# Performance work log

Hardware: AMD Instinct MI355X
Metric: run time of the kernel (lower is better)

The kernel has to match this reference:

```python
import jax, jax.numpy as jnp
import numpy as np
import math

B, T, D = 2, 2048, 2048
H, HKV, HD = 16, 4, 128
THETA = 10000.0


def _rope_tables(seq_len, head_dim, theta):
    inv_freq = 1.0 / theta ** (jnp.arange(0, head_dim, 2, dtype=jnp.float32) / head_dim)
    t = jnp.arange(seq_len, dtype=jnp.float32)
    freqs = jnp.outer(t, inv_freq)  # (T, HD/2)
    return jnp.cos(freqs), jnp.sin(freqs)


def _apply_rope(x, cos, sin):
    # x: (B, h, T, HD); cos/sin: (T, HD/2)
    hd = x.shape[-1]
    x1, x2 = x[..., : hd // 2], x[..., hd // 2 :]
    rotated = jnp.concatenate([-x2, x1], axis=-1)
    c = jnp.concatenate([cos, cos], axis=-1)[None, None]  # (1,1,T,HD)
    s = jnp.concatenate([sin, sin], axis=-1)[None, None]
    return x * c + rotated * s


def setup_inputs() -> dict:
    key = jax.random.key(0)
    ks = jax.random.split(key, 5)
    sc = 0.02
    return {
        "x": jax.random.normal(ks[0], (B, T, D), dtype=jnp.float32),
        "attention_mask": jnp.ones((B, T), dtype=jnp.int32),
        "causal": 1,
        "wq": jax.random.normal(ks[1], (D, H * HD), dtype=jnp.float32) * sc,
        "wk": jax.random.normal(ks[2], (D, HKV * HD), dtype=jnp.float32) * sc,
        "wv": jax.random.normal(ks[3], (D, HKV * HD), dtype=jnp.float32) * sc,
        "wo": jax.random.normal(ks[4], (D, D), dtype=jnp.float32) * sc,
    }


def reference(x, attention_mask, causal, wq, wk, wv, wo):
    b, t, d = x.shape
    G = H // HKV  # query heads per kv head

    q = (x @ wq).reshape(b, t, H, HD).transpose(0, 2, 1, 3)      # (B,H,T,HD)
    k = (x @ wk).reshape(b, t, HKV, HD).transpose(0, 2, 1, 3)    # (B,HKV,T,HD)
    v = (x @ wv).reshape(b, t, HKV, HD).transpose(0, 2, 1, 3)

    cos, sin = _rope_tables(t, HD, THETA)
    q = _apply_rope(q, cos, sin)
    k = _apply_rope(k, cos, sin)

    # group queries so repeat_interleave of k/v is implicit
    qg = q.reshape(b, HKV, G, t, HD)
    scores = jnp.einsum("bkgtd,bksd->bkgts", qg, k) / math.sqrt(HD)

    key_pad = (attention_mask == 0)[:, None, None, None, :]  # (B,1,1,1,T)
    scores = jnp.where(key_pad, -jnp.inf, scores)
    if causal:
        cm = jnp.triu(jnp.ones((t, t), dtype=bool), k=1)
        scores = jnp.where(cm[None, None, None], -jnp.inf, scores)

    attn = jax.nn.softmax(scores, axis=-1)  # dropout p=0.0 -> identity in eval
    out = jnp.einsum("bkgts,bksd->bkgtd", attn, v)            # (B,HKV,G,T,HD)
    out = out.reshape(b, H, t, HD).transpose(0, 2, 1, 3).reshape(b, t, H * HD)
    return out @ wo
```

## Files before the change

### kernel.cpp

```cpp
#include <hip/hip_runtime.h>
#include <hip/hip_bf16.h>
#include <stdint.h>

#define B_    2
#define T_    2048
#define D_    2048
#define H_    16
#define HKV_  4
#define HD_   128
#define BT_   (B_ * T_)
#define QD_   2048
#define KVD_  512

typedef float  f32x4 __attribute__((ext_vector_type(4)));
typedef short  s16x8 __attribute__((ext_vector_type(8)));
typedef unsigned short us;

__device__ __forceinline__ us f2bf(float f) {
    unsigned int u = __builtin_bit_cast(unsigned int, f);
    u += 0x7FFFu + ((u >> 16) & 1u);
    return (us)(u >> 16);
}
__device__ __forceinline__ float bf2f(us s) {
    unsigned int u = ((unsigned int)s) << 16;
    return __builtin_bit_cast(float, u);
}
__device__ __forceinline__ unsigned pack2(float a, float b) {
    return (unsigned)f2bf(a) | ((unsigned)f2bf(b) << 16);
}

#define GLOBAL_AS __attribute__((address_space(1)))
#define LDS_AS    __attribute__((address_space(3)))

__device__ __forceinline__ void gload16(const void* g, void* l) {
    __builtin_amdgcn_global_load_lds((const GLOBAL_AS uint32_t*)g,
                                     (LDS_AS uint32_t*)l, 16, 0, 0);
}

__global__ __launch_bounds__(256)
void wtrans(const float* __restrict__ w, us* __restrict__ wt, int K, int N) {
    __shared__ float t[32][33];
    const int k0 = blockIdx.x * 32, n0 = blockIdx.y * 32;
    const int tid = threadIdx.x;
    const int r = tid >> 3, c4 = (tid & 7) << 2;
    const float4 v = *(const float4*)&w[(size_t)(k0 + r) * N + n0 + c4];
    t[r][c4 + 0] = v.x; t[r][c4 + 1] = v.y; t[r][c4 + 2] = v.z; t[r][c4 + 3] = v.w;
    __syncthreads();
    ushort4 o;
    o.x = f2bf(t[c4 + 0][r]); o.y = f2bf(t[c4 + 1][r]);
    o.z = f2bf(t[c4 + 2][r]); o.w = f2bf(t[c4 + 3][r]);
    *(ushort4*)&wt[(size_t)(n0 + r) * K + k0 + c4] = o;
}

__global__ __launch_bounds__(256)
void cvt_bf16(const float* __restrict__ x, us* __restrict__ xb, int n8) {
    const int i = blockIdx.x * 256 + threadIdx.x;
    if (i >= n8) return;
    const float4 a = ((const float4*)x)[i * 2];
    const float4 b = ((const float4*)x)[i * 2 + 1];
    s16x8 o;
    o[0] = (short)f2bf(a.x); o[1] = (short)f2bf(a.y);
    o[2] = (short)f2bf(a.z); o[3] = (short)f2bf(a.w);
    o[4] = (short)f2bf(b.x); o[5] = (short)f2bf(b.y);
    o[6] = (short)f2bf(b.z); o[7] = (short)f2bf(b.w);
    *(s16x8*)&xb[(size_t)i * 8] = o;
}

__global__ __launch_bounds__(256)
void build_tabs(float* __restrict__ tab, float* __restrict__ bias,
                const int* __restrict__ amask) {
    const int i = blockIdx.x * 256 + threadIdx.x;
    if (i < T_ * 64) {
        const int t = i >> 6, f = i & 63;
        const float inv = __expf((float)f * (-0.14391156642478335f));
        float s, c;
        sincosf((float)t * inv, &s, &c);
        tab[t * 128 + f] = c;
        tab[t * 128 + 64 + f] = s;
    }
    if (i < B_ * T_) bias[i] = amask[i] ? 0.f : -__builtin_inff();
}

template <int NH>
__global__ __launch_bounds__(256)
void rope_apply(us* __restrict__ x, const float* __restrict__ tab, int total4) {
    const int idx = blockIdx.x * 256 + threadIdx.x;
    if (idx >= total4) return;
    const int i0  = (idx & 15) << 2;
    const int rest = idx >> 4;
    const int h   = rest % NH;
    const int row = rest / NH;
    const int t   = row & (T_ - 1);
    const f32x4 c = *(const f32x4*)&tab[t * 128 + i0];
    const f32x4 s = *(const f32x4*)&tab[t * 128 + 64 + i0];
    const size_t base = (size_t)row * (NH * 128) + h * 128 + i0;
    ushort4 lo = *(ushort4*)&x[base];
    ushort4 hi = *(ushort4*)&x[base + 64];
    float x1[4] = {bf2f(lo.x), bf2f(lo.y), bf2f(lo.z), bf2f(lo.w)};
    float x2[4] = {bf2f(hi.x), bf2f(hi.y), bf2f(hi.z), bf2f(hi.w)};
    ushort4 olo, ohi;
    olo.x = f2bf(x1[0]*c[0] - x2[0]*s[0]); ohi.x = f2bf(x2[0]*c[0] + x1[0]*s[0]);
    olo.y = f2bf(x1[1]*c[1] - x2[1]*s[1]); ohi.y = f2bf(x2[1]*c[1] + x1[1]*s[1]);
    olo.z = f2bf(x1[2]*c[2] - x2[2]*s[2]); ohi.z = f2bf(x2[2]*c[2] + x1[2]*s[2]);
    olo.w = f2bf(x1[3]*c[3] - x2[3]*s[3]); ohi.w = f2bf(x2[3]*c[3] + x1[3]*s[3]);
    *(ushort4*)&x[base]      = olo;
    *(ushort4*)&x[base + 64] = ohi;
}

template <bool AF32, int OUTMODE>
__global__ __launch_bounds__(256)
void gemm_bf16(const void* __restrict__ Ap, const us* __restrict__ Bt,
               void* __restrict__ Cp, int M, int N, int K) {
    __shared__ us As[128 * 32];
    __shared__ us Bs[128 * 32];

    const int tid  = threadIdx.x;
    const int lane = tid & 63;
    const int w    = tid >> 6;
    const int lrow = lane & 15;
    const int lhi  = lane >> 4;
    const int wm   = w >> 1;
    const int wn   = w & 1;
    const int mbase = blockIdx.y * 128;
    const int nbase = blockIdx.x * 128;

    f32x4 acc[4][4] = {};

    for (int k0 = 0; k0 < K; k0 += 32) {
        __syncthreads();
        if constexpr (AF32) {
            const float* A = (const float*)Ap;
#pragma unroll
            for (int i = 0; i < 2; ++i) {
                const int c   = tid * 2 + i;
                const int row = c >> 2, cc = c & 3;
                const float* src = A + (size_t)(mbase + row) * K + k0 + ((cc ^ (row & 3)) << 3);
                const float4 v0 = *(const float4*)src;
                const float4 v1 = *(const float4*)(src + 4);
                s16x8 o;
                o[0] = (short)f2bf(v0.x); o[1] = (short)f2bf(v0.y);
                o[2] = (short)f2bf(v0.z); o[3] = (short)f2bf(v0.w);
                o[4] = (short)f2bf(v1.x); o[5] = (short)f2bf(v1.y);
                o[6] = (short)f2bf(v1.z); o[7] = (short)f2bf(v1.w);
                *(s16x8*)&As[c * 8] = o;
            }
        } else {
            const us* A = (const us*)Ap;
#pragma unroll
            for (int i = 0; i < 2; ++i) {
                const int cb = i * 256 + w * 64;
                const int c  = cb + lane;
                const int row = c >> 2, cc = c & 3;
                gload16(A + (size_t)(mbase + row) * K + k0 + ((cc ^ (row & 3)) << 3),
                        &As[cb * 8]);
            }
        }
#pragma unroll
        for (int i = 0; i < 2; ++i) {
            const int cb = i * 256 + w * 64;
            const int c  = cb + lane;
            const int row = c >> 2, cc = c & 3;
            gload16(Bt + (size_t)(nbase + row) * K + k0 + ((cc ^ (row & 3)) << 3),
                    &Bs[cb * 8]);
        }
        __syncthreads();

        s16x8 af[4], bfv[4];
#pragma unroll
        for (int mi = 0; mi < 4; ++mi) {
            const int r = wm * 64 + mi * 16 + lrow;
            af[mi] = *(const s16x8*)&As[r * 32 + ((lhi ^ (r & 3)) << 3)];
        }
#pragma unroll
        for (int ni = 0; ni < 4; ++ni) {
            const int r = wn * 64 + ni * 16 + lrow;
            bfv[ni] = *(const s16x8*)&Bs[r * 32 + ((lhi ^ (r & 3)) << 3)];
        }
#pragma unroll
        for (int mi = 0; mi < 4; ++mi)
#pragma unroll
            for (int ni = 0; ni < 4; ++ni)
                acc[mi][ni] = __builtin_amdgcn_mfma_f32_16x16x32_bf16(
                    af[mi], bfv[ni], acc[mi][ni], 0, 0, 0);
    }

#pragma unroll
    for (int mi = 0; mi < 4; ++mi) {
#pragma unroll
        for (int ni = 0; ni < 4; ++ni) {
#pragma unroll
            for (int r = 0; r < 4; ++r) {
                const int gm = mbase + wm * 64 + mi * 16 + lhi * 4 + r;
                const int gn = nbase + wn * 64 + ni * 16 + lrow;
                const float v = acc[mi][ni][r];
                if constexpr (OUTMODE == 0) {
                    ((us*)Cp)[(size_t)gm * N + gn] = f2bf(v);
                } else if constexpr (OUTMODE == 1) {
                    ((float*)Cp)[(size_t)gm * N + gn] = v;
                } else {
                    const int b = gm >> 11, t = gm & (T_ - 1);
                    if (gn < KVD_) {
                        ((us*)Cp)[(size_t)gm * KVD_ + gn] = f2bf(v);
                    } else {
                        const int nv = gn - KVD_;
                        us* vt = (us*)Cp + (size_t)BT_ * KVD_;
                        vt[((size_t)(b * HKV_ + (nv >> 7)) * 128 + (nv & 127)) * T_ + t] = f2bf(v);
                    }
                }
            }
        }
    }
}

__global__ __launch_bounds__(256)
void attn_mfma2(const us* __restrict__ qg, const us* __restrict__ kg,
                const us* __restrict__ vtg, const float* __restrict__ bias,
                const int* __restrict__ causal_p, us* __restrict__ outg) {
    __shared__ us lds[32768];

    const int q0 = blockIdx.x * 64;
    const int h  = blockIdx.y;
    const int b  = blockIdx.z;
    const int kvh = h >> 2;
    const int causal = *causal_p;
    const int tid  = threadIdx.x;
    const int lane = tid & 63;
    const int w    = tid >> 6;
    const int lrow = lane & 15, lhi = lane >> 4;

    auto stageKV = [&](int buf, int s0) {
        us* Kd = lds + buf * 8192;
        us* Vd = lds + 16384 + buf * 8192;
#pragma unroll
        for (int i = 0; i < 4; ++i) {
            const int cb = i * 256 + w * 64;
            const int c  = cb + lane;
            const int row = c >> 4, cc = c & 15;
            gload16(kg + (size_t)(b * T_ + s0 + row) * KVD_ + kvh * HD_ + ((cc ^ (row & 7)) << 3),
                    Kd + cb * 8);
        }
#pragma unroll
        for (int i = 0; i < 4; ++i) {
            const int cb = i * 256 + w * 64;
            const int c  = cb + lane;
            const int row = c >> 3, cc = c & 7;
            gload16(vtg + (size_t)((b * HKV_ + kvh) * 128 + row) * T_ + s0 + ((cc ^ (row & 7)) << 3),
                    Vd + cb * 8);
        }
    };

#pragma unroll
    for (int i = 0; i < 4; ++i) {
        const int cb = i * 256 + w * 64;
        const int c  = cb + lane;
        const int row = c >> 4, cc = c & 15;
        gload16(qg + (size_t)(b * T_ + q0 + row) * QD_ + h * HD_ + ((cc ^ (row & 7)) << 3),
                lds + 8192 + cb * 8);
    }
    __syncthreads();

    s16x8 qf[4];
    {
        const us* Qsp = lds + 8192;
        const int qr = w * 16 + lrow;
#pragma unroll
        for (int kc = 0; kc < 4; ++kc)
            qf[kc] = *(const s16x8*)&Qsp[qr * 128 + (((kc * 4 + lhi) ^ (qr & 7)) << 3)];
    }
    stageKV(0, 0);
    __syncthreads();

    f32x4 o[8] = {};
    float m_run = -__builtin_inff();
    float l_run = 0.f;
    const int qp = q0 + w * 16 + lrow;
    const int smax = causal ? (q0 + 64) : T_;
    const int ntiles = smax >> 6;
    const float rscale = 0.08838834764831845f;
    int cur = 0;

    for (int it = 0; it < ntiles; ++it) {
        const int s0 = it << 6;
        if (it + 1 < ntiles) stageKV(cur ^ 1, s0 + 64);

        const us* Kcur = lds + cur * 8192;
        const us* Vcur = lds + 16384 + cur * 8192;

        f32x4 sf[4];
#pragma unroll
        for (int j = 0; j < 4; ++j) {
            f32x4 s = {0.f, 0.f, 0.f, 0.f};
            const int kr = j * 16 + lrow;
#pragma unroll
            for (int kc = 0; kc < 4; ++kc) {
                const s16x8 kf = *(const s16x8*)&Kcur[kr * 128 + (((kc * 4 + lhi) ^ (kr & 7)) << 3)];
                s = __builtin_amdgcn_mfma_f32_16x16x32_bf16(kf, qf[kc], s, 0, 0, 0);
            }
            sf[j] = s;
        }

        const float* brow = bias + b * T_ + s0;
        f32x4 bv[4];
#pragma unroll
        for (int j = 0; j < 4; ++j)
            bv[j] = *(const f32x4*)&brow[j * 16 + lhi * 4];
        const bool needc = causal && (s0 + 63 > q0 + w * 16);
        float x[4][4];
#pragma unroll
        for (int j = 0; j < 4; ++j)
#pragma unroll
            for (int r = 0; r < 4; ++r) {
                float xv = sf[j][r] * rscale + bv[j][r];
                if (needc && (s0 + j * 16 + lhi * 4 + r > qp)) xv = -__builtin_inff();
                x[j][r] = xv;
            }

        float tmax = x[0][0];
#pragma unroll
        for (int j = 0; j < 4; ++j)
#pragma unroll
            for (int r = 0; r < 4; ++r) tmax = fmaxf(tmax, x[j][r]);
        tmax = fmaxf(tmax, __shfl_xor(tmax, 16));
        tmax = fmaxf(tmax, __shfl_xor(tmax, 32));
        const float mn = fmaxf(m_run, tmax);
        float corr, ls = 0.f, ps[4][4];
        if (mn == -__builtin_inff()) {
            corr = 1.f;
#pragma unroll
            for (int j = 0; j < 4; ++j)
#pragma unroll
                for (int r = 0; r < 4; ++r) ps[j][r] = 0.f;
        } else {
            corr = __expf(m_run - mn);
#pragma unroll
            for (int j = 0; j < 4; ++j)
#pragma unroll
                for (int r = 0; r < 4; ++r) { ps[j][r] = __expf(x[j][r] - mn); ls += ps[j][r]; }
        }
        ls += __shfl_xor(ls, 16);
        ls += __shfl_xor(ls, 32);
        l_run = l_run * corr + ls;
        m_run = mn;

        const unsigned w00 = pack2(ps[0][0], ps[0][1]), w01 = pack2(ps[0][2], ps[0][3]);
        const unsigned w10 = pack2(ps[1][0], ps[1][1]), w11 = pack2(ps[1][2], ps[1][3]);
        const unsigned w20 = pack2(ps[2][0], ps[2][1]), w21 = pack2(ps[2][2], ps[2][3]);
        const unsigned w30 = pack2(ps[3][0], ps[3][1]), w31 = pack2(ps[3][2], ps[3][3]);
        int a0w[4], a1w[4];
#pragma unroll
        for (int m = 0; m < 4; ++m) {
            const int src = lrow + ((lhi & 1) << 5) + ((m & 2) << 3);
            const unsigned c0 = (m & 1) ? w01 : w00;
            const unsigned c1 = (m & 1) ? w11 : w10;
            const int t0 = __shfl((int)c0, src);
            const int t1 = __shfl((int)c1, src);
            a0w[m] = (lhi & 2) ? t1 : t0;
            const unsigned c2 = (m & 1) ? w21 : w20;
            const unsigned c3 = (m & 1) ? w31 : w30;
            const int t2 = __shfl((int)c2, src);
            const int t3 = __shfl((int)c3, src);
            a1w[m] = (lhi & 2) ? t3 : t2;
        }
        const s16x8 a0 = __builtin_bit_cast(s16x8, make_int4(a0w[0], a0w[1], a0w[2], a0w[3]));
        const s16x8 a1 = __builtin_bit_cast(s16x8, make_int4(a1w[0], a1w[1], a1w[2], a1w[3]));

        float co[4];
#pragma unroll
        for (int r = 0; r < 4; ++r) co[r] = __shfl(corr, lhi * 4 + r);
#pragma unroll
        for (int dc = 0; dc < 8; ++dc) {
            o[dc][0] *= co[0]; o[dc][1] *= co[1];
            o[dc][2] *= co[2]; o[dc][3] *= co[3];
        }
#pragma unroll
        for (int dc = 0; dc < 8; ++dc) {
            const int vr = dc * 16 + lrow;
            const s16x8 vb0 = *(const s16x8*)&Vcur[vr * 64 + ((lhi ^ (vr & 7)) << 3)];
            o[dc] = __builtin_amdgcn_mfma_f32_16x16x32_bf16(a0, vb0, o[dc], 0, 0, 0);
            const s16x8 vb1 = *(const s16x8*)&Vcur[vr * 64 + (((4 + lhi) ^ (vr & 7)) << 3)];
            o[dc] = __builtin_amdgcn_mfma_f32_16x16x32_bf16(a1, vb1, o[dc], 0, 0, 0);
        }
        __syncthreads();
        cur ^= 1;
    }

    float lq[4];
#pragma unroll
    for (int r = 0; r < 4; ++r) lq[r] = __shfl(l_run, lhi * 4 + r);
#pragma unroll
    for (int r = 0; r < 4; ++r) {
        const float invl = lq[r] > 0.f ? 1.0f / lq[r] : 0.f;
        const size_t base = (size_t)(b * T_ + q0 + w * 16 + lhi * 4 + r) * QD_ + h * HD_ + lrow;
#pragma unroll
        for (int dc = 0; dc < 8; ++dc)
            outg[base + dc * 16] = f2bf(o[dc][r] * invl);
    }
}

extern "C" void kernel_launch(void* const* d_in, const int* in_sizes, int n_in,
                              void* d_out, int out_size, void* d_ws, size_t ws_size,
                              hipStream_t stream) {
    const float* x      = (const float*)d_in[0];
    const int*   amask  = (const int*)d_in[1];
    const int*   causal = (const int*)d_in[2];
    const float* wq     = (const float*)d_in[3];
    const float* wk     = (const float*)d_in[4];
    const float* wv     = (const float*)d_in[5];
    const float* wo     = (const float*)d_in[6];
    float* out = (float*)d_out;

    us* p    = (us*)d_ws;
    us* wqt  = p;  p += (size_t)QD_ * D_;
    us* wkvt = p;  p += (size_t)1024 * D_;
    us* qb   = p;  p += (size_t)BT_ * QD_;
    us* kb   = p;  p += (size_t)BT_ * KVD_;
    us* vt   = p;  p += (size_t)BT_ * KVD_;
    float* tab  = (float*)p;  p += (size_t)T_ * 128 * 2;
    float* bias = (float*)p;  p += (size_t)B_ * T_ * 2;
    us* xw   = p;

    const size_t need_xb = ((size_t)(p - (us*)d_ws) + (size_t)BT_ * D_) * sizeof(us);
    const bool useXB = ws_size >= need_xb;

    build_tabs<<<512, 256, 0, stream>>>(tab, bias, amask);
    wtrans<<<dim3(64, 64), 256, 0, stream>>>(wq, wqt, D_, QD_);
    wtrans<<<dim3(64, 16), 256, 0, stream>>>(wk, wkvt, D_, KVD_);
    wtrans<<<dim3(64, 16), 256, 0, stream>>>(wv, wkvt + (size_t)KVD_ * D_, D_, KVD_);

    if (useXB) {
        cvt_bf16<<<4096, 256, 0, stream>>>(x, xw, BT_ * D_ / 8);
        gemm_bf16<false, 0><<<dim3(16, 32), 256, 0, stream>>>(xw, wqt, qb, BT_, QD_, D_);
        gemm_bf16<false, 2><<<dim3(8, 32), 256, 0, stream>>>(xw, wkvt, kb, BT_, 1024, D_);
    } else {
        gemm_bf16<true, 0><<<dim3(16, 32), 256, 0, stream>>>(x, wqt, qb, BT_, QD_, D_);
        gemm_bf16<true, 2><<<dim3(8, 32), 256, 0, stream>>>(x, wkvt, kb, BT_, 1024, D_);
    }

    rope_apply<H_><<<4096, 256, 0, stream>>>(qb, tab, BT_ * H_ * 16);
    rope_apply<HKV_><<<1024, 256, 0, stream>>>(kb, tab, BT_ * HKV_ * 16);

    attn_mfma2<<<dim3(32, 16, 2), 256, 0, stream>>>(qb, kb, vt, bias, causal, qb);

    wtrans<<<dim3(64, 64), 256, 0, stream>>>(wo, xw, D_, D_);
    gemm_bf16<false, 1><<<dim3(16, 32), 256, 0, stream>>>(qb, xw, out, BT_, D_, D_);
}
```

Before: 458.2 us.

## Double attention query tile to 128 rows with deferred rescale and LDS P transpose

```diff
diff --git a/kernel.cpp b/kernel.cpp
--- a/kernel.cpp
+++ b/kernel.cpp
@@ -188,24 +188,29 @@
     for (int mi = 0; mi < 4; ++mi) {
 #pragma unroll
         for (int ni = 0; ni < 4; ++ni) {
-#pragma unroll
-            for (int r = 0; r < 4; ++r) {
-                const int gm = mbase + wm * 64 + mi * 16 + lhi * 4 + r;
-                const int gn = nbase + wn * 64 + ni * 16 + lrow;
-                const float v = acc[mi][ni][r];
-                if constexpr (OUTMODE == 0) {
-                    ((us*)Cp)[(size_t)gm * N + gn] = f2bf(v);
-                } else if constexpr (OUTMODE == 1) {
-                    ((float*)Cp)[(size_t)gm * N + gn] = v;
+            const int gm0 = mbase + wm * 64 + mi * 16 + lhi * 4;
+            const int gn  = nbase + wn * 64 + ni * 16 + lrow;
+            if constexpr (OUTMODE == 0) {
+#pragma unroll
+                for (int r = 0; r < 4; ++r)
+                    ((us*)Cp)[(size_t)(gm0 + r) * N + gn] = f2bf(acc[mi][ni][r]);
+            } else if constexpr (OUTMODE == 1) {
+#pragma unroll
+                for (int r = 0; r < 4; ++r)
+                    ((float*)Cp)[(size_t)(gm0 + r) * N + gn] = acc[mi][ni][r];
+            } else {
+                if (gn < KVD_) {
+#pragma unroll
+                    for (int r = 0; r < 4; ++r)
+                        ((us*)Cp)[(size_t)(gm0 + r) * KVD_ + gn] = f2bf(acc[mi][ni][r]);
                 } else {
-                    const int b = gm >> 11, t = gm & (T_ - 1);
-                    if (gn < KVD_) {
-                        ((us*)Cp)[(size_t)gm * KVD_ + gn] = f2bf(v);
-                    } else {
-                        const int nv = gn - KVD_;
-                        us* vt = (us*)Cp + (size_t)BT_ * KVD_;
-                        vt[((size_t)(b * HKV_ + (nv >> 7)) * 128 + (nv & 127)) * T_ + t] = f2bf(v);
-                    }
+                    const int nv = gn - KVD_;
+                    const int bb = gm0 >> 11, t = gm0 & (T_ - 1);
+                    us* vt = (us*)Cp + (size_t)BT_ * KVD_;
+                    ushort4 o4;
+                    o4.x = f2bf(acc[mi][ni][0]); o4.y = f2bf(acc[mi][ni][1]);
+                    o4.z = f2bf(acc[mi][ni][2]); o4.w = f2bf(acc[mi][ni][3]);
+                    *(ushort4*)&vt[((size_t)(bb * HKV_ + (nv >> 7)) * 128 + (nv & 127)) * T_ + t] = o4;
                 }
             }
         }
@@ -213,12 +218,13 @@
 }
 
 __global__ __launch_bounds__(256)
-void attn_mfma2(const us* __restrict__ qg, const us* __restrict__ kg,
+void attn_mfma3(const us* __restrict__ qg, const us* __restrict__ kg,
                 const us* __restrict__ vtg, const float* __restrict__ bias,
                 const int* __restrict__ causal_p, us* __restrict__ outg) {
-    __shared__ us lds[32768];
-
-    const int q0 = blockIdx.x * 64;
+    __shared__ us lds[40960];
+
+    const int qt = 15 - blockIdx.x;
+    const int q0 = qt * 128;
     const int h  = blockIdx.y;
     const int b  = blockIdx.z;
     const int kvh = h >> 2;
@@ -250,32 +256,34 @@
     };
 
 #pragma unroll
-    for (int i = 0; i < 4; ++i) {
+    for (int i = 0; i < 8; ++i) {
         const int cb = i * 256 + w * 64;
         const int c  = cb + lane;
         const int row = c >> 4, cc = c & 15;
+        us* dst = (cb < 1024) ? (lds + 8192 + cb * 8) : (lds + 24576 + (cb - 1024) * 8);
         gload16(qg + (size_t)(b * T_ + q0 + row) * QD_ + h * HD_ + ((cc ^ (row & 7)) << 3),
-                lds + 8192 + cb * 8);
+                dst);
     }
     __syncthreads();
 
-    s16x8 qf[4];
-    {
-        const us* Qsp = lds + 8192;
-        const int qr = w * 16 + lrow;
+    s16x8 qf[2][4];
+#pragma unroll
+    for (int s = 0; s < 2; ++s) {
+        const int qr = w * 32 + s * 16 + lrow;
+        const us* Qsp = (w * 32 + s * 16 < 64) ? (lds + 8192 + qr * 128)
+                                               : (lds + 24576 + (qr - 64) * 128);
 #pragma unroll
         for (int kc = 0; kc < 4; ++kc)
-            qf[kc] = *(const s16x8*)&Qsp[qr * 128 + (((kc * 4 + lhi) ^ (qr & 7)) << 3)];
+            qf[s][kc] = *(const s16x8*)&Qsp[((kc * 4 + lhi) ^ (qr & 7)) << 3];
     }
     stageKV(0, 0);
     __syncthreads();
 
-    f32x4 o[8] = {};
-    float m_run = -__builtin_inff();
-    float l_run = 0.f;
-    const int qp = q0 + w * 16 + lrow;
-    const int smax = causal ? (q0 + 64) : T_;
-    const int ntiles = smax >> 6;
+    f32x4 o[2][8] = {};
+    float m_run[2] = {-__builtin_inff(), -__builtin_inff()};
+    float l_run[2] = {0.f, 0.f};
+    us* Pw = lds + 32768 + w * 2048;
+    const int ntiles = (causal ? (q0 + 128) : T_) >> 6;
     const float rscale = 0.08838834764831845f;
     int cur = 0;
 
@@ -286,17 +294,18 @@
         const us* Kcur = lds + cur * 8192;
         const us* Vcur = lds + 16384 + cur * 8192;
 
-        f32x4 sf[4];
+        f32x4 sf[2][4];
 #pragma unroll
         for (int j = 0; j < 4; ++j) {
-            f32x4 s = {0.f, 0.f, 0.f, 0.f};
+            f32x4 a0 = {0.f, 0.f, 0.f, 0.f}, a1 = {0.f, 0.f, 0.f, 0.f};
             const int kr = j * 16 + lrow;
 #pragma unroll
             for (int kc = 0; kc < 4; ++kc) {
                 const s16x8 kf = *(const s16x8*)&Kcur[kr * 128 + (((kc * 4 + lhi) ^ (kr & 7)) << 3)];
-                s = __builtin_amdgcn_mfma_f32_16x16x32_bf16(kf, qf[kc], s, 0, 0, 0);
-            }
-            sf[j] = s;
+                a0 = __builtin_amdgcn_mfma_f32_16x16x32_bf16(kf, qf[0][kc], a0, 0, 0, 0);
+                a1 = __builtin_amdgcn_mfma_f32_16x16x32_bf16(kf, qf[1][kc], a1, 0, 0, 0);
+            }
+            sf[0][j] = a0; sf[1][j] = a1;
         }
 
         const float* brow = bias + b * T_ + s0;
@@ -304,96 +313,108 @@
 #pragma unroll
         for (int j = 0; j < 4; ++j)
             bv[j] = *(const f32x4*)&brow[j * 16 + lhi * 4];
-        const bool needc = causal && (s0 + 63 > q0 + w * 16);
-        float x[4][4];
-#pragma unroll
-        for (int j = 0; j < 4; ++j)
-#pragma unroll
-            for (int r = 0; r < 4; ++r) {
-                float xv = sf[j][r] * rscale + bv[j][r];
-                if (needc && (s0 + j * 16 + lhi * 4 + r > qp)) xv = -__builtin_inff();
-                x[j][r] = xv;
-            }
-
-        float tmax = x[0][0];
-#pragma unroll
-        for (int j = 0; j < 4; ++j)
-#pragma unroll
-            for (int r = 0; r < 4; ++r) tmax = fmaxf(tmax, x[j][r]);
-        tmax = fmaxf(tmax, __shfl_xor(tmax, 16));
-        tmax = fmaxf(tmax, __shfl_xor(tmax, 32));
-        const float mn = fmaxf(m_run, tmax);
-        float corr, ls = 0.f, ps[4][4];
-        if (mn == -__builtin_inff()) {
-            corr = 1.f;
+
+        s16x8 pa[2][2];
+#pragma unroll
+        for (int s = 0; s < 2; ++s) {
+            const int qp = q0 + w * 32 + s * 16 + lrow;
+            const bool needc = causal && (s0 + 63 > q0 + w * 32 + s * 16);
+            float x[4][4];
 #pragma unroll
             for (int j = 0; j < 4; ++j)
 #pragma unroll
-                for (int r = 0; r < 4; ++r) ps[j][r] = 0.f;
-        } else {
-            corr = __expf(m_run - mn);
+                for (int r = 0; r < 4; ++r) {
+                    float xv = sf[s][j][r] * rscale + bv[j][r];
+                    if (needc && (s0 + j * 16 + lhi * 4 + r > qp)) xv = -__builtin_inff();
+                    x[j][r] = xv;
+                }
+
+            float tmax = x[0][0];
 #pragma unroll
             for (int j = 0; j < 4; ++j)
 #pragma unroll
-                for (int r = 0; r < 4; ++r) { ps[j][r] = __expf(x[j][r] - mn); ls += ps[j][r]; }
-        }
-        ls += __shfl_xor(ls, 16);
-        ls += __shfl_xor(ls, 32);
-        l_run = l_run * corr + ls;
-        m_run = mn;
-
-        const unsigned w00 = pack2(ps[0][0], ps[0][1]), w01 = pack2(ps[0][2], ps[0][3]);
-        const unsigned w10 = pack2(ps[1][0], ps[1][1]), w11 = pack2(ps[1][2], ps[1][3]);
-        const unsigned w20 = pack2(ps[2][0], ps[2][1]), w21 = pack2(ps[2][2], ps[2][3]);
-        const unsigned w30 = pack2(ps[3][0], ps[3][1]), w31 = pack2(ps[3][2], ps[3][3]);
-        int a0w[4], a1w[4];
-#pragma unroll
-        for (int m = 0; m < 4; ++m) {
-            const int src = lrow + ((lhi & 1) << 5) + ((m & 2) << 3);
-            const unsigned c0 = (m & 1) ? w01 : w00;
-            const unsigned c1 = (m & 1) ? w11 : w10;
-            const int t0 = __shfl((int)c0, src);
-            const int t1 = __shfl((int)c1, src);
-            a0w[m] = (lhi & 2) ? t1 : t0;
-            const unsigned c2 = (m & 1) ? w21 : w20;
-            const unsigned c3 = (m & 1) ? w31 : w30;
-            const int t2 = __shfl((int)c2, src);
-            const int t3 = __shfl((int)c3, src);
-            a1w[m] = (lhi & 2) ? t3 : t2;
-        }
-        const s16x8 a0 = __builtin_bit_cast(s16x8, make_int4(a0w[0], a0w[1], a0w[2], a0w[3]));
-        const s16x8 a1 = __builtin_bit_cast(s16x8, make_int4(a1w[0], a1w[1], a1w[2], a1w[3]));
-
-        float co[4];
-#pragma unroll
-        for (int r = 0; r < 4; ++r) co[r] = __shfl(corr, lhi * 4 + r);
-#pragma unroll
-        for (int dc = 0; dc < 8; ++dc) {
-            o[dc][0] *= co[0]; o[dc][1] *= co[1];
-            o[dc][2] *= co[2]; o[dc][3] *= co[3];
-        }
+                for (int r = 0; r < 4; ++r) tmax = fmaxf(tmax, x[j][r]);
+            tmax = fmaxf(tmax, __shfl_xor(tmax, 16));
+            tmax = fmaxf(tmax, __shfl_xor(tmax, 32));
+
+            const bool defer = (m_run[s] != -__builtin_inff()) &&
+                               __all(tmax <= m_run[s] + 8.f);
+            float corr = 1.f, ls = 0.f;
+            float ps[4][4];
+            if (defer) {
+                const float mo = m_run[s];
+#pragma unroll
+                for (int j = 0; j < 4; ++j)
+#pragma unroll
+                    for (int r = 0; r < 4; ++r) { ps[j][r] = __expf(x[j][r] - mo); ls += ps[j][r]; }
+            } else {
+                const float mn = fmaxf(m_run[s], tmax);
+                if (mn == -__builtin_inff()) {
+#pragma unroll
+                    for (int j = 0; j < 4; ++j)
+#pragma unroll
+                        for (int r = 0; r < 4; ++r) ps[j][r] = 0.f;
+                } else {
+                    corr = __expf(m_run[s] - mn);
+#pragma unroll
+                    for (int j = 0; j < 4; ++j)
+#pragma unroll
+                        for (int r = 0; r < 4; ++r) { ps[j][r] = __expf(x[j][r] - mn); ls += ps[j][r]; }
+                }
+                float co[4];
+#pragma unroll
+                for (int r = 0; r < 4; ++r) co[r] = __shfl(corr, lhi * 4 + r);
+#pragma unroll
+                for (int dc = 0; dc < 8; ++dc) {
+                    o[s][dc][0] *= co[0]; o[s][dc][1] *= co[1];
+                    o[s][dc][2] *= co[2]; o[s][dc][3] *= co[3];
+                }
+                m_run[s] = mn;
+            }
+            ls += __shfl_xor(ls, 16);
+            ls += __shfl_xor(ls, 32);
+            l_run[s] = l_run[s] * corr + ls;
+
+            us* Ps = Pw + s * 1024;
+#pragma unroll
+            for (int j = 0; j < 4; ++j) {
+                uint2 wv;
+                wv.x = pack2(ps[j][0], ps[j][1]);
+                wv.y = pack2(ps[j][2], ps[j][3]);
+                *(uint2*)&Ps[lrow * 64 + ((16 * j + 4 * lhi) ^ ((lrow & 7) << 3))] = wv;
+            }
+            pa[s][0] = *(const s16x8*)&Ps[lrow * 64 + ((8 * lhi) ^ ((lrow & 7) << 3))];
+            pa[s][1] = *(const s16x8*)&Ps[lrow * 64 + ((32 + 8 * lhi) ^ ((lrow & 7) << 3))];
+        }
+
 #pragma unroll
         for (int dc = 0; dc < 8; ++dc) {
             const int vr = dc * 16 + lrow;
             const s16x8 vb0 = *(const s16x8*)&Vcur[vr * 64 + ((lhi ^ (vr & 7)) << 3)];
-            o[dc] = __builtin_amdgcn_mfma_f32_16x16x32_bf16(a0, vb0, o[dc], 0, 0, 0);
             const s16x8 vb1 = *(const s16x8*)&Vcur[vr * 64 + (((4 + lhi) ^ (vr & 7)) << 3)];
-            o[dc] = __builtin_amdgcn_mfma_f32_16x16x32_bf16(a1, vb1, o[dc], 0, 0, 0);
+            o[0][dc] = __builtin_amdgcn_mfma_f32_16x16x32_bf16(pa[0][0], vb0, o[0][dc], 0, 0, 0);
+            o[0][dc] = __builtin_amdgcn_mfma_f32_16x16x32_bf16(pa[0][1], vb1, o[0][dc], 0, 0, 0);
+            o[1][dc] = __builtin_amdgcn_mfma_f32_16x16x32_bf16(pa[1][0], vb0, o[1][dc], 0, 0, 0);
+            o[1][dc] = __builtin_amdgcn_mfma_f32_16x16x32_bf16(pa[1][1], vb1, o[1][dc], 0, 0, 0);
         }
         __syncthreads();
         cur ^= 1;
     }
 
-    float lq[4];
-#pragma unroll
-    for (int r = 0; r < 4; ++r) lq[r] = __shfl(l_run, lhi * 4 + r);
-#pragma unroll
-    for (int r = 0; r < 4; ++r) {
-        const float invl = lq[r] > 0.f ? 1.0f / lq[r] : 0.f;
-        const size_t base = (size_t)(b * T_ + q0 + w * 16 + lhi * 4 + r) * QD_ + h * HD_ + lrow;
-#pragma unroll
-        for (int dc = 0; dc < 8; ++dc)
-            outg[base + dc * 16] = f2bf(o[dc][r] * invl);
+#pragma unroll
+    for (int s = 0; s < 2; ++s) {
+        float lq[4];
+#pragma unroll
+        for (int r = 0; r < 4; ++r) lq[r] = __shfl(l_run[s], lhi * 4 + r);
+#pragma unroll
+        for (int r = 0; r < 4; ++r) {
+            const float invl = lq[r] > 0.f ? 1.0f / lq[r] : 0.f;
+            const size_t base =
+                (size_t)(b * T_ + q0 + w * 32 + s * 16 + lhi * 4 + r) * QD_ + h * HD_ + lrow;
+#pragma unroll
+            for (int dc = 0; dc < 8; ++dc)
+                outg[base + dc * 16] = f2bf(o[s][dc][r] * invl);
+        }
     }
 }
 
@@ -439,7 +460,7 @@
     rope_apply<H_><<<4096, 256, 0, stream>>>(qb, tab, BT_ * H_ * 16);
     rope_apply<HKV_><<<1024, 256, 0, stream>>>(kb, tab, BT_ * HKV_ * 16);
 
-    attn_mfma2<<<dim3(32, 16, 2), 256, 0, stream>>>(qb, kb, vt, bias, causal, qb);
+    attn_mfma3<<<dim3(16, 16, 2), 256, 0, stream>>>(qb, kb, vt, bias, causal, qb);
 
     wtrans<<<dim3(64, 64), 256, 0, stream>>>(wo, xw, D_, D_);
     gemm_bf16<false, 1><<<dim3(16, 32), 256, 0, stream>>>(qb, xw, out, BT_, D_, D_);
```

Measured after the change: 466.8 us. No clear change (+1.9%).
